# Performance work log

Hardware: AMD Instinct MI355X
Metric: run time of the kernel (lower is better)

## Reference

```python
import jax, jax.numpy as jnp
import numpy as np

EMBED = 128
HEADS = 8
HEAD_DIM = EMBED // HEADS

def setup_inputs() -> dict:
    key = jax.random.key(0)
    ks = jax.random.split(key, 8)
    B, N = 2, 4096
    values = jax.random.normal(ks[0], (B, N, EMBED), dtype=jnp.float32)
    keys = jax.random.normal(ks[1], (B, N, EMBED), dtype=jnp.float32)
    query = jax.random.normal(ks[2], (B, N, EMBED), dtype=jnp.float32)
    s = 1.0 / np.sqrt(HEAD_DIM)
    Wv = jax.random.normal(ks[3], (HEAD_DIM, HEAD_DIM), dtype=jnp.float32) * s
    Wk = jax.random.normal(ks[4], (HEAD_DIM, HEAD_DIM), dtype=jnp.float32) * s
    Wq = jax.random.normal(ks[5], (HEAD_DIM, HEAD_DIM), dtype=jnp.float32) * s
    Wo = jax.random.normal(ks[6], (EMBED, EMBED), dtype=jnp.float32) * (1.0 / np.sqrt(EMBED))
    bo = jnp.zeros((EMBED,), dtype=jnp.float32)
    return {"values": values, "keys": keys, "query": query,
            "Wv": Wv, "Wk": Wk, "Wq": Wq, "Wo": Wo, "bo": bo}

def reference(values, keys, query, Wv, Wk, Wq, Wo, bo):
    B, N, _ = query.shape
    # split heads: [B,N,H,Dh]
    v = values.reshape(B, N, HEADS, HEAD_DIM)
    k = keys.reshape(B, N, HEADS, HEAD_DIM)
    q = query.reshape(B, N, HEADS, HEAD_DIM)
    # per-head linear (torch Linear: x @ W.T), same weight for all heads
    v = jnp.einsum('bnhd,ed->bnhe', v, Wv)
    k = jnp.einsum('bnhd,ed->bnhe', k, Wk)
    q = jnp.einsum('bnhd,ed->bnhe', q, Wq)
    # scores [B,H,N,N], note scale by sqrt(embed_size) as in original
    energy = jnp.einsum('bqhd,bkhd->bhqk', q, k) / jnp.sqrt(jnp.float32(EMBED))
    attn = jax.nn.softmax(energy, axis=-1)
    out = jnp.einsum('bhql,blhd->bqhd', attn, v).reshape(B, N, EMBED)
    return out @ Wo.T + bo
```

## Files before the change

### kernel.cpp

```cpp
#include <hip/hip_runtime.h>

#define BB 2
#define NN 4096
#define HH 8
#define DD 16
#define EE 128
#define LBLK 64
#define QBLK 128
#define NTILES (NN / LBLK)
#define KROW 20
#define VROW 72
#define KBUF (LBLK * KROW)
#define VBUF (DD * VROW)

typedef _Float16 f16;
typedef _Float16 f16x4 __attribute__((ext_vector_type(4)));
typedef _Float16 f16x2 __attribute__((ext_vector_type(2)));
typedef float f32x4 __attribute__((ext_vector_type(4)));

#define QSCALE 0.12751741f

__global__ __launch_bounds__(256) void proj_kernel(
    const float* __restrict__ vals, const float* __restrict__ keys,
    const float* __restrict__ query,
    const float* __restrict__ Wv, const float* __restrict__ Wk,
    const float* __restrict__ Wq,
    f16* __restrict__ Qp, f16* __restrict__ Kp, f16* __restrict__ Vt)
{
    __shared__ float W[256];
    const int p = blockIdx.x >> 8;
    const float* Wsrc = (p == 0) ? Wv : ((p == 1) ? Wk : Wq);
    W[threadIdx.x] = Wsrc[threadIdx.x];
    __syncthreads();

    const int idx = ((blockIdx.x & 255) << 8) | threadIdx.x;
    const int n = idx & 4095;
    const int h = (idx >> 12) & 7;
    const int b = idx >> 15;

    const float* xsrc = (p == 0) ? vals : ((p == 1) ? keys : query);
    const float4* xp = (const float4*)(xsrc + (size_t)(b * NN + n) * EE + h * DD);
    const float4 x0 = xp[0], x1 = xp[1], x2 = xp[2], x3 = xp[3];
    const float scale = (p == 2) ? QSCALE : 1.0f;

    alignas(16) f16 out[16];
    #pragma unroll
    for (int e = 0; e < 16; e++) {
        const float4* wr = (const float4*)(W + e * 16);
        const float4 w0 = wr[0], w1 = wr[1], w2 = wr[2], w3 = wr[3];
        float acc = x0.x * w0.x + x0.y * w0.y + x0.z * w0.z + x0.w * w0.w
                  + x1.x * w1.x + x1.y * w1.y + x1.z * w1.z + x1.w * w1.w
                  + x2.x * w2.x + x2.y * w2.y + x2.z * w2.z + x2.w * w2.w
                  + x3.x * w3.x + x3.y * w3.y + x3.z * w3.z + x3.w * w3.w;
        out[e] = (f16)(acc * scale);
    }

    if (p == 0) {
        f16* dst = Vt + (size_t)(b * HH + h) * DD * NN + n;
        #pragma unroll
        for (int e = 0; e < 16; e++) dst[(size_t)e * NN] = out[e];
    } else {
        f16* dst = ((p == 1) ? Kp : Qp) + (size_t)((b * HH + h) * NN + n) * DD;
        ((uint4*)dst)[0] = ((const uint4*)out)[0];
        ((uint4*)dst)[1] = ((const uint4*)out)[1];
    }
}

__global__ __launch_bounds__(256) void wo_conv(const float* __restrict__ Wo,
                                               f16* __restrict__ Wo16)
{
    const int i = blockIdx.x * 256 + threadIdx.x;
    Wo16[i] = (f16)Wo[i];
}

__global__ __launch_bounds__(512) void attn_kernel(
    const f16* __restrict__ Qp, const f16* __restrict__ Kp,
    const f16* __restrict__ Vt, f16* __restrict__ Of)
{
    __shared__ f16 Kl[2 * KBUF];
    __shared__ f16 Vl[2 * VBUF];

    const int tid = threadIdx.x;
    const int lane = tid & 63;
    const int wave = tid >> 6;
    const int r = lane & 15;
    const int g = lane >> 4;
    const int bh = blockIdx.x >> 5;
    const int q0 = (blockIdx.x & 31) * QBLK + wave * 16;

    const bool stK = tid < 256;
    const f16* gptr;
    f16* wbase;
    int wstep;
    size_t gstep;
    if (stK) {
        const int row = tid >> 2, c4 = (tid & 3) << 2;
        gptr = Kp + ((size_t)bh * NN + row) * DD + c4;
        wbase = Kl + row * KROW + c4;
        wstep = KBUF;
        gstep = (size_t)LBLK * DD;
    } else {
        const int u = tid & 255;
        const int row = u >> 4, c4 = (u & 15) << 2;
        gptr = Vt + ((size_t)(bh * DD + row)) * NN + c4;
        wbase = Vl + row * VROW + c4;
        wstep = VBUF;
        gstep = (size_t)LBLK;
    }

    const f16x4 qf = *(const f16x4*)(Qp + ((size_t)bh * NN + q0 + r) * DD + 4 * g);

    {
        f16x4 sreg = *(const f16x4*)gptr;
        gptr += gstep;
        *(f16x4*)wbase = sreg;
    }
    __syncthreads();

    f32x4 acc0 = {0.f, 0.f, 0.f, 0.f}, acc1 = {0.f, 0.f, 0.f, 0.f};
    float d0 = 0.f, d1 = 0.f;
    int cur = 0;

    const int kread = r * KROW + 4 * g;
    const int vread = r * VROW + 4 * g;

    for (int t = 0; t < NTILES; ++t) {
        f16x4 sreg;
        if (t < NTILES - 1) {
            sreg = *(const f16x4*)gptr;
            gptr += gstep;
        }

        const f16* Kb = Kl + cur * KBUF;
        const f16* Vb = Vl + cur * VBUF;

        #pragma unroll
        for (int c = 0; c < 4; ++c) {
            const f16x4 kf = *(const f16x4*)(Kb + kread + 16 * c * KROW);
            f32x4 st = {0.f, 0.f, 0.f, 0.f};
            st = __builtin_amdgcn_mfma_f32_16x16x16f16(kf, qf, st, 0, 0, 0);
            const float p0 = __builtin_amdgcn_exp2f(st[0]);
            const float p1 = __builtin_amdgcn_exp2f(st[1]);
            const float p2 = __builtin_amdgcn_exp2f(st[2]);
            const float p3 = __builtin_amdgcn_exp2f(st[3]);
            const f16x2 lo = __builtin_bit_cast(f16x2, __builtin_amdgcn_cvt_pkrtz(p0, p1));
            const f16x2 hi = __builtin_bit_cast(f16x2, __builtin_amdgcn_cvt_pkrtz(p2, p3));
            const f16x4 pf = __builtin_shufflevector(lo, hi, 0, 1, 2, 3);
            const f16x4 vf = *(const f16x4*)(Vb + vread + 16 * c);
            if (c & 1) {
                d1 += (p0 + p1) + (p2 + p3);
                acc1 = __builtin_amdgcn_mfma_f32_16x16x16f16(vf, pf, acc1, 0, 0, 0);
            } else {
                d0 += (p0 + p1) + (p2 + p3);
                acc0 = __builtin_amdgcn_mfma_f32_16x16x16f16(vf, pf, acc0, 0, 0, 0);
            }
        }

        if (t < NTILES - 1) {
            *(f16x4*)(wbase + (cur ^ 1) * wstep) = sreg;
        }
        __syncthreads();
        cur ^= 1;
    }

    float denom = d0 + d1;
    denom += __shfl_xor(denom, 16, 64);
    denom += __shfl_xor(denom, 32, 64);
    const float inv = 1.0f / denom;
    const f32x4 acc = acc0 + acc1;

    const int b = bh >> 3, h = bh & 7;
    f16x4 o;
    o[0] = (f16)(acc[0] * inv);
    o[1] = (f16)(acc[1] * inv);
    o[2] = (f16)(acc[2] * inv);
    o[3] = (f16)(acc[3] * inv);
    *(f16x4*)(Of + (size_t)(b * NN + q0 + r) * EE + h * DD + 4 * g) = o;
}

__global__ __launch_bounds__(256) void outproj_kernel(
    const f16* __restrict__ Of, const f16* __restrict__ Wo16,
    const float* __restrict__ bo, float* __restrict__ out)
{
    const int lane = threadIdx.x & 63;
    const int wave = threadIdx.x >> 6;
    const int r = lane & 15;
    const int g = lane >> 4;
    const int n0 = (blockIdx.x * 2 + (wave >> 1)) * 16;
    const int eh = (wave & 1) * 4;

    f32x4 acc[4];
    #pragma unroll
    for (int e = 0; e < 4; e++) acc[e] = (f32x4){0.f, 0.f, 0.f, 0.f};

    #pragma unroll
    for (int k0 = 0; k0 < 8; k0++) {
        const f16x4 a = *(const f16x4*)(Of + (size_t)(n0 + r) * EE + k0 * 16 + 4 * g);
        #pragma unroll
        for (int e = 0; e < 4; e++) {
            const f16x4 bf = *(const f16x4*)(Wo16 + (size_t)((eh + e) * 16 + r) * EE + k0 * 16 + 4 * g);
            acc[e] = __builtin_amdgcn_mfma_f32_16x16x16f16(a, bf, acc[e], 0, 0, 0);
        }
    }

    #pragma unroll
    for (int e = 0; e < 4; e++) {
        const float bias = bo[(eh + e) * 16 + r];
        #pragma unroll
        for (int i = 0; i < 4; i++) {
            out[(size_t)(n0 + 4 * g + i) * EE + (eh + e) * 16 + r] = acc[e][i] + bias;
        }
    }
}

extern "C" void kernel_launch(void* const* d_in, const int* in_sizes, int n_in,
                              void* d_out, int out_size, void* d_ws, size_t ws_size,
                              hipStream_t stream)
{
    const float* vals  = (const float*)d_in[0];
    const float* keys  = (const float*)d_in[1];
    const float* query = (const float*)d_in[2];
    const float* Wv    = (const float*)d_in[3];
    const float* Wk    = (const float*)d_in[4];
    const float* Wq    = (const float*)d_in[5];
    const float* Wo    = (const float*)d_in[6];
    const float* bo    = (const float*)d_in[7];
    float* out = (float*)d_out;

    char* w = (char*)d_ws;
    f16* Qp   = (f16*)(w);
    f16* Kp   = (f16*)(w + (2u << 20));
    f16* Vt   = (f16*)(w + (4u << 20));
    f16* Of   = (f16*)(w + (6u << 20));
    f16* Wo16 = (f16*)(w + (8u << 20));

    hipLaunchKernelGGL(proj_kernel, dim3(768), dim3(256), 0, stream,
                       vals, keys, query, Wv, Wk, Wq, Qp, Kp, Vt);
    hipLaunchKernelGGL(wo_conv, dim3(64), dim3(256), 0, stream, Wo, Wo16);
    hipLaunchKernelGGL(attn_kernel, dim3(512), dim3(512), 0, stream,
                       Qp, Kp, Vt, Of);
    hipLaunchKernelGGL(outproj_kernel, dim3(256), dim3(256), 0, stream,
                       Of, Wo16, bo, out);
}
```

Before: 62.56 us.

## Split attention key range across two blocks and merge partials in out-projection

The attention kernel now splits the key sequence into two halves, launching twice as many blocks. Each block writes unnormalized fp32 partial outputs and row denominators to workspace, and the out-projection kernel sums the halves and normalizes. The Wo fp16 conversion is folded into the projection launch, which saves one kernel launch. Shared memory now uses an MFMA-fragment-ordered layout so each lane reads K/V with a single 16-byte load per pair of chunks, and the denominator uses fdot2. This trades extra fp32 partial-output traffic for better occupancy and shorter per-block serial loops.

Measured after the change: 60.41 us. 3.4% less time.

```diff
diff --git a/kernel.cpp b/kernel.cpp
--- a/kernel.cpp
+++ b/kernel.cpp
@@ -7,15 +7,13 @@
 #define EE 128
 #define LBLK 64
 #define QBLK 128
-#define NTILES (NN / LBLK)
-#define KROW 20
-#define VROW 72
-#define KBUF (LBLK * KROW)
-#define VBUF (DD * VROW)
+#define NTH 32
 
 typedef _Float16 f16;
 typedef _Float16 f16x4 __attribute__((ext_vector_type(4)));
 typedef _Float16 f16x2 __attribute__((ext_vector_type(2)));
+typedef _Float16 f16x8 __attribute__((ext_vector_type(8)));
+typedef __fp16 h16x2 __attribute__((ext_vector_type(2)));
 typedef float f32x4 __attribute__((ext_vector_type(4)));
 
 #define QSCALE 0.12751741f
@@ -24,9 +22,15 @@
     const float* __restrict__ vals, const float* __restrict__ keys,
     const float* __restrict__ query,
     const float* __restrict__ Wv, const float* __restrict__ Wk,
-    const float* __restrict__ Wq,
-    f16* __restrict__ Qp, f16* __restrict__ Kp, f16* __restrict__ Vt)
-{
+    const float* __restrict__ Wq, const float* __restrict__ Wo,
+    f16* __restrict__ Qp, f16* __restrict__ Kp, f16* __restrict__ Vt,
+    f16* __restrict__ Wo16)
+{
+    if (blockIdx.x >= 768) {
+        const int i = (blockIdx.x - 768) * 256 + threadIdx.x;
+        Wo16[i] = (f16)Wo[i];
+        return;
+    }
     __shared__ float W[256];
     const int p = blockIdx.x >> 8;
     const float* Wsrc = (p == 0) ? Wv : ((p == 1) ? Wk : Wq);
@@ -66,121 +70,127 @@
     }
 }
 
-__global__ __launch_bounds__(256) void wo_conv(const float* __restrict__ Wo,
-                                               f16* __restrict__ Wo16)
-{
-    const int i = blockIdx.x * 256 + threadIdx.x;
-    Wo16[i] = (f16)Wo[i];
-}
-
 __global__ __launch_bounds__(512) void attn_kernel(
     const f16* __restrict__ Qp, const f16* __restrict__ Kp,
-    const f16* __restrict__ Vt, f16* __restrict__ Of)
-{
-    __shared__ f16 Kl[2 * KBUF];
-    __shared__ f16 Vl[2 * VBUF];
+    const f16* __restrict__ Vt, float* __restrict__ Oacc,
+    float* __restrict__ den)
+{
+    __shared__ f16 Kl[2][LBLK * DD];
+    __shared__ f16 Vl[2][LBLK * DD];
 
     const int tid = threadIdx.x;
     const int lane = tid & 63;
     const int wave = tid >> 6;
     const int r = lane & 15;
     const int g = lane >> 4;
-    const int bh = blockIdx.x >> 5;
-    const int q0 = (blockIdx.x & 31) * QBLK + wave * 16;
-
+
+    const int bid = blockIdx.x;
+    const int half = bid & 1;
+    const int qt = (bid >> 1) & 31;
+    const int bh = bid >> 6;
+    const int q0 = qt * QBLK + wave * 16;
+    const int L0 = half * (NN / 2);
+
+    const int u = tid & 255;
+    const int c01 = u >> 7;
+    const int sl = (u & 127) >> 1;
+    const int clo = u & 1;
+    const int sr = sl & 15;
+    const int sg = sl >> 4;
     const bool stK = tid < 256;
     const f16* gptr;
-    f16* wbase;
-    int wstep;
     size_t gstep;
     if (stK) {
-        const int row = tid >> 2, c4 = (tid & 3) << 2;
-        gptr = Kp + ((size_t)bh * NN + row) * DD + c4;
-        wbase = Kl + row * KROW + c4;
-        wstep = KBUF;
+        gptr = Kp + ((size_t)bh * NN + L0 + 16 * (2 * c01 + clo) + sr) * DD + 4 * sg;
         gstep = (size_t)LBLK * DD;
     } else {
-        const int u = tid & 255;
-        const int row = u >> 4, c4 = (u & 15) << 2;
-        gptr = Vt + ((size_t)(bh * DD + row)) * NN + c4;
-        wbase = Vl + row * VROW + c4;
-        wstep = VBUF;
+        gptr = Vt + ((size_t)bh * DD + sr) * NN + L0 + 16 * (2 * c01 + clo) + 4 * sg;
         gstep = (size_t)LBLK;
     }
+    f16* wdst = (stK ? &Kl[0][0] : &Vl[0][0]) + u * 4;
 
     const f16x4 qf = *(const f16x4*)(Qp + ((size_t)bh * NN + q0 + r) * DD + 4 * g);
 
     {
         f16x4 sreg = *(const f16x4*)gptr;
         gptr += gstep;
-        *(f16x4*)wbase = sreg;
+        *(f16x4*)wdst = sreg;
     }
     __syncthreads();
 
-    f32x4 acc0 = {0.f, 0.f, 0.f, 0.f}, acc1 = {0.f, 0.f, 0.f, 0.f};
-    float d0 = 0.f, d1 = 0.f;
+    f32x4 acc0 = {0.f,0.f,0.f,0.f}, acc1 = {0.f,0.f,0.f,0.f};
+    f32x4 acc2 = {0.f,0.f,0.f,0.f}, acc3 = {0.f,0.f,0.f,0.f};
+    float d0 = 0.f, d1 = 0.f, d2 = 0.f, d3 = 0.f;
+    const h16x2 ones = {(__fp16)1.0f, (__fp16)1.0f};
     int cur = 0;
 
-    const int kread = r * KROW + 4 * g;
-    const int vread = r * VROW + 4 * g;
-
-    for (int t = 0; t < NTILES; ++t) {
+#define CHUNK(KF, VF, ACC, DEN) { \
+    f32x4 st = {0.f,0.f,0.f,0.f}; \
+    st = __builtin_amdgcn_mfma_f32_16x16x16f16((KF), qf, st, 0, 0, 0); \
+    const float p0 = __builtin_amdgcn_exp2f(st[0]); \
+    const float p1 = __builtin_amdgcn_exp2f(st[1]); \
+    const float p2 = __builtin_amdgcn_exp2f(st[2]); \
+    const float p3 = __builtin_amdgcn_exp2f(st[3]); \
+    const h16x2 lo = __builtin_amdgcn_cvt_pkrtz(p0, p1); \
+    const h16x2 hi = __builtin_amdgcn_cvt_pkrtz(p2, p3); \
+    DEN = __builtin_amdgcn_fdot2(lo, ones, DEN, false); \
+    DEN = __builtin_amdgcn_fdot2(hi, ones, DEN, false); \
+    const f16x4 pf = __builtin_shufflevector( \
+        __builtin_bit_cast(f16x2, lo), __builtin_bit_cast(f16x2, hi), 0, 1, 2, 3); \
+    ACC = __builtin_amdgcn_mfma_f32_16x16x16f16((VF), pf, ACC, 0, 0, 0); }
+
+    for (int t = 0; t < NTH; ++t) {
         f16x4 sreg;
-        if (t < NTILES - 1) {
+        if (t < NTH - 1) {
             sreg = *(const f16x4*)gptr;
             gptr += gstep;
         }
 
-        const f16* Kb = Kl + cur * KBUF;
-        const f16* Vb = Vl + cur * VBUF;
-
-        #pragma unroll
-        for (int c = 0; c < 4; ++c) {
-            const f16x4 kf = *(const f16x4*)(Kb + kread + 16 * c * KROW);
-            f32x4 st = {0.f, 0.f, 0.f, 0.f};
-            st = __builtin_amdgcn_mfma_f32_16x16x16f16(kf, qf, st, 0, 0, 0);
-            const float p0 = __builtin_amdgcn_exp2f(st[0]);
-            const float p1 = __builtin_amdgcn_exp2f(st[1]);
-            const float p2 = __builtin_amdgcn_exp2f(st[2]);
-            const float p3 = __builtin_amdgcn_exp2f(st[3]);
-            const f16x2 lo = __builtin_bit_cast(f16x2, __builtin_amdgcn_cvt_pkrtz(p0, p1));
-            const f16x2 hi = __builtin_bit_cast(f16x2, __builtin_amdgcn_cvt_pkrtz(p2, p3));
-            const f16x4 pf = __builtin_shufflevector(lo, hi, 0, 1, 2, 3);
-            const f16x4 vf = *(const f16x4*)(Vb + vread + 16 * c);
-            if (c & 1) {
-                d1 += (p0 + p1) + (p2 + p3);
-                acc1 = __builtin_amdgcn_mfma_f32_16x16x16f16(vf, pf, acc1, 0, 0, 0);
-            } else {
-                d0 += (p0 + p1) + (p2 + p3);
-                acc0 = __builtin_amdgcn_mfma_f32_16x16x16f16(vf, pf, acc0, 0, 0, 0);
-            }
-        }
-
-        if (t < NTILES - 1) {
-            *(f16x4*)(wbase + (cur ^ 1) * wstep) = sreg;
+        const f16* Kb = &Kl[cur][0];
+        const f16* Vb = &Vl[cur][0];
+        const f16x8 kA = *(const f16x8*)(Kb + lane * 8);
+        const f16x8 kB = *(const f16x8*)(Kb + 512 + lane * 8);
+        const f16x8 vA = *(const f16x8*)(Vb + lane * 8);
+        const f16x8 vB = *(const f16x8*)(Vb + 512 + lane * 8);
+        const f16x4 kf0 = __builtin_shufflevector(kA, kA, 0, 1, 2, 3);
+        const f16x4 kf1 = __builtin_shufflevector(kA, kA, 4, 5, 6, 7);
+        const f16x4 kf2 = __builtin_shufflevector(kB, kB, 0, 1, 2, 3);
+        const f16x4 kf3 = __builtin_shufflevector(kB, kB, 4, 5, 6, 7);
+        const f16x4 vf0 = __builtin_shufflevector(vA, vA, 0, 1, 2, 3);
+        const f16x4 vf1 = __builtin_shufflevector(vA, vA, 4, 5, 6, 7);
+        const f16x4 vf2 = __builtin_shufflevector(vB, vB, 0, 1, 2, 3);
+        const f16x4 vf3 = __builtin_shufflevector(vB, vB, 4, 5, 6, 7);
+
+        CHUNK(kf0, vf0, acc0, d0)
+        CHUNK(kf1, vf1, acc1, d1)
+        CHUNK(kf2, vf2, acc2, d2)
+        CHUNK(kf3, vf3, acc3, d3)
+
+        if (t < NTH - 1) {
+            *(f16x4*)(wdst + (cur ^ 1) * (LBLK * DD)) = sreg;
         }
         __syncthreads();
         cur ^= 1;
     }
-
-    float denom = d0 + d1;
-    denom += __shfl_xor(denom, 16, 64);
-    denom += __shfl_xor(denom, 32, 64);
-    const float inv = 1.0f / denom;
-    const f32x4 acc = acc0 + acc1;
+#undef CHUNK
+
+    float dt = (d0 + d1) + (d2 + d3);
+    dt += __shfl_xor(dt, 16, 64);
+    dt += __shfl_xor(dt, 32, 64);
+    const f32x4 acc = (acc0 + acc1) + (acc2 + acc3);
 
     const int b = bh >> 3, h = bh & 7;
-    f16x4 o;
-    o[0] = (f16)(acc[0] * inv);
-    o[1] = (f16)(acc[1] * inv);
-    o[2] = (f16)(acc[2] * inv);
-    o[3] = (f16)(acc[3] * inv);
-    *(f16x4*)(Of + (size_t)(b * NN + q0 + r) * EE + h * DD + 4 * g) = o;
+    float* OaccH = Oacc + (size_t)half * (BB * NN * EE);
+    *(f32x4*)(OaccH + ((size_t)(b * NN + q0 + r)) * EE + h * DD + 4 * g) = acc;
+    if (lane < 16) {
+        den[(size_t)(half * 16 + bh) * NN + q0 + lane] = dt;
+    }
 }
 
 __global__ __launch_bounds__(256) void outproj_kernel(
-    const f16* __restrict__ Of, const f16* __restrict__ Wo16,
-    const float* __restrict__ bo, float* __restrict__ out)
+    const float* __restrict__ Oacc, const float* __restrict__ den,
+    const f16* __restrict__ Wo16, const float* __restrict__ bo,
+    float* __restrict__ out)
 {
     const int lane = threadIdx.x & 63;
     const int wave = threadIdx.x >> 6;
@@ -189,13 +199,29 @@
     const int n0 = (blockIdx.x * 2 + (wave >> 1)) * 16;
     const int eh = (wave & 1) * 4;
 
+    const int n = n0 + r;
+    const int b = n >> 12;
+    const int nn = n & 4095;
+    const float* Oa0 = Oacc + (size_t)n * EE;
+    const float* Oa1 = Oacc + (size_t)(BB * NN * EE) + (size_t)n * EE;
+
     f32x4 acc[4];
     #pragma unroll
     for (int e = 0; e < 4; e++) acc[e] = (f32x4){0.f, 0.f, 0.f, 0.f};
 
     #pragma unroll
     for (int k0 = 0; k0 < 8; k0++) {
-        const f16x4 a = *(const f16x4*)(Of + (size_t)(n0 + r) * EE + k0 * 16 + 4 * g);
+        const size_t didx = (size_t)(b * 8 + k0) * NN + nn;
+        const float inv = 1.0f / (den[didx] + den[(size_t)16 * NN + didx]);
+        const f32x4 xa = *(const f32x4*)(Oa0 + k0 * 16 + 4 * g);
+        const f32x4 xb = *(const f32x4*)(Oa1 + k0 * 16 + 4 * g);
+        const float s0 = (xa[0] + xb[0]) * inv;
+        const float s1 = (xa[1] + xb[1]) * inv;
+        const float s2 = (xa[2] + xb[2]) * inv;
+        const float s3 = (xa[3] + xb[3]) * inv;
+        const f16x4 a = __builtin_shufflevector(
+            __builtin_bit_cast(f16x2, __builtin_amdgcn_cvt_pkrtz(s0, s1)),
+            __builtin_bit_cast(f16x2, __builtin_amdgcn_cvt_pkrtz(s2, s3)), 0, 1, 2, 3);
         #pragma unroll
         for (int e = 0; e < 4; e++) {
             const f16x4 bf = *(const f16x4*)(Wo16 + (size_t)((eh + e) * 16 + r) * EE + k0 * 16 + 4 * g);
@@ -228,17 +254,17 @@
     float* out = (float*)d_out;
 
     char* w = (char*)d_ws;
-    f16* Qp   = (f16*)(w);
-    f16* Kp   = (f16*)(w + (2u << 20));
-    f16* Vt   = (f16*)(w + (4u << 20));
-    f16* Of   = (f16*)(w + (6u << 20));
-    f16* Wo16 = (f16*)(w + (8u << 20));
-
-    hipLaunchKernelGGL(proj_kernel, dim3(768), dim3(256), 0, stream,
-                       vals, keys, query, Wv, Wk, Wq, Qp, Kp, Vt);
-    hipLaunchKernelGGL(wo_conv, dim3(64), dim3(256), 0, stream, Wo, Wo16);
-    hipLaunchKernelGGL(attn_kernel, dim3(512), dim3(512), 0, stream,
-                       Qp, Kp, Vt, Of);
+    f16*   Qp   = (f16*)(w);
+    f16*   Kp   = (f16*)(w + (2u << 20));
+    f16*   Vt   = (f16*)(w + (4u << 20));
+    f16*   Wo16 = (f16*)(w + (6u << 20));
+    float* den  = (float*)(w + (6u << 20) + 65536);
+    float* Oacc = (float*)(w + (7u << 20));
+
+    hipLaunchKernelGGL(proj_kernel, dim3(832), dim3(256), 0, stream,
+                       vals, keys, query, Wv, Wk, Wq, Wo, Qp, Kp, Vt, Wo16);
+    hipLaunchKernelGGL(attn_kernel, dim3(1024), dim3(512), 0, stream,
+                       Qp, Kp, Vt, Oacc, den);
     hipLaunchKernelGGL(outproj_kernel, dim3(256), dim3(256), 0, stream,
-                       Of, Wo16, bo, out);
-}
+                       Oacc, den, Wo16, bo, out);
+}
```
